# Kernel tuning notes

Measured on AMD Instinct MI355X. Metric: run time of the kernel, lower is better.

## Reference

```python
import jax, jax.numpy as jnp
import numpy as np

N = 8192
E = 262144
H = 64


def setup_inputs() -> dict:
    key = jax.random.key(0)
    ks = jax.random.split(key, 9)
    edge_index = jax.random.randint(ks[0], (2, E), 0, N, dtype=jnp.int64)
    edge_attr = jax.random.uniform(ks[1], (E,), dtype=jnp.float32)
    node_features = jax.random.normal(ks[2], (N, N), dtype=jnp.float32)
    # GCNConv weights (glorot-ish scale) and biases
    W1 = jax.random.normal(ks[3], (N, H), dtype=jnp.float32) / np.sqrt(N)
    b1 = jnp.zeros((H,), dtype=jnp.float32)
    W2 = jax.random.normal(ks[4], (H, H), dtype=jnp.float32) / np.sqrt(H)
    b2 = jnp.zeros((H,), dtype=jnp.float32)
    fcW = jax.random.normal(ks[5], (H, N), dtype=jnp.float32) / np.sqrt(H)
    fcb = jnp.zeros((N,), dtype=jnp.float32)
    return {"edge_index": edge_index, "edge_attr": edge_attr,
            "node_features": node_features,
            "W1": W1, "b1": b1, "W2": W2, "b2": b2,
            "fcW": fcW, "fcb": fcb}


def _gcn_conv(x, W, b, src, dst, ew, n_nodes):
    # PyG GCNConv with edge weights: x' = D^{-1/2} (A + I) D^{-1/2} (x W) + b
    # src/dst/ew already include self-loops (weight 1.0).
    x = x @ W                                        # [N, out]
    deg = jax.ops.segment_sum(ew, dst, num_segments=n_nodes)  # in-degree w/ loops
    dinv = jax.lax.rsqrt(deg)                        # deg >= 1 due to self loops
    norm = dinv[src] * ew * dinv[dst]                # [E+N]
    out = jax.ops.segment_sum(x[src] * norm[:, None], dst, num_segments=n_nodes)
    return out + b


def reference(edge_index, edge_attr, node_features, W1, b1, W2, b2, fcW, fcb):
    n_nodes = node_features.shape[0]
    loops = jnp.arange(n_nodes, dtype=edge_index.dtype)
    src = jnp.concatenate([edge_index[0], loops])
    dst = jnp.concatenate([edge_index[1], loops])
    ew = jnp.concatenate([edge_attr, jnp.ones((n_nodes,), edge_attr.dtype)])
    x = jax.nn.relu(_gcn_conv(node_features, W1, b1, src, dst, ew, n_nodes))
    x = jax.nn.relu(_gcn_conv(x, W2, b2, src, dst, ew, n_nodes))
    x = x @ fcW + fcb
    return jax.nn.softmax(x, axis=-1)
```

## Files before the change

### kernel.cpp

```cpp
#include <hip/hip_runtime.h>


#define NN 8192
#define NE 262144
#define HD 64
#define KCH 1024
#define NKC 8
#define NTS (KCH/64)

typedef float f32x4 __attribute__((ext_vector_type(4)));
typedef short v8s   __attribute__((ext_vector_type(8)));
typedef unsigned short ushort_t;

__device__ __forceinline__ unsigned short bf16_rne(float f){
  union { float f; unsigned u; } v; v.f = f;
  unsigned r = v.u + 0x7fffu + ((v.u >> 16) & 1u);
  return (unsigned short)(r >> 16);
}
__device__ __forceinline__ float bf16_f32(unsigned short h){
  union { unsigned u; float f; } v; v.u = ((unsigned)h) << 16;
  return v.f;
}
__device__ __forceinline__ f32x4 mfma16(v8s a, v8s b, f32x4 c){
  return __builtin_amdgcn_mfma_f32_16x16x32_bf16(a, b, c, 0, 0, 0);
}
__device__ __forceinline__ void gload16(const void* g, void* l){
  __builtin_amdgcn_global_load_lds(
      (const __attribute__((address_space(1))) unsigned int*)g,
      (__attribute__((address_space(3))) unsigned int*)l, 16, 0, 0);
}

__global__ __launch_bounds__(256) void k_xcast(const float* __restrict__ X,
                                               ushort_t* __restrict__ xb){
  size_t i = ((size_t)blockIdx.x*256 + threadIdx.x)*8;
  f32x4 a = *(const f32x4*)(X + i);
  f32x4 b = *(const f32x4*)(X + i + 4);
  v8s o;
  #pragma unroll
  for (int j=0;j<4;++j){
    o[j]   = (short)bf16_rne(a[j]);
    o[4+j] = (short)bf16_rne(b[j]);
  }
  *(v8s*)(xb + i) = o;
}

__global__ void k_prep0(const float* __restrict__ W1, const float* __restrict__ fcW,
                        ushort_t* w1hi, ushort_t* fcwp,
                        float* deg, int* cnt, int* wcnt, float* S){
  int idx = blockIdx.x*blockDim.x + threadIdx.x;
  if (idx < NN){ deg[idx]=1.0f; cnt[idx]=0; wcnt[idx]=0; S[idx]=0.0f; }
  {
    int kk = idx & 31, c = (idx>>5)&15, nt = (idx>>9)&3, kb = idx>>11;
    int k = kb*32 + kk, col = nt*16 + c;
    float w = W1[(size_t)k*HD + col];
    int chunk = idx >> 3, e = idx & 7;
    int sidx = ((chunk ^ (c & 7)) << 3) | e;
    w1hi[sidx] = bf16_rne(w);
  }
  {
    int kk = idx & 31, c = (idx>>5)&15, cblk = (idx>>9)&511, kb = idx>>18;
    int k = kb*32 + kk, col = cblk*16 + c;
    fcwp[idx] = bf16_rne(fcW[(size_t)k*NN + col]);
  }
}

__global__ void k_deg_cnt(const int* ei, const float* ew, float* deg, int* cnt){
  int e = blockIdx.x*blockDim.x + threadIdx.x;
  if (e < NE){
    int d = ei[NE + e];
    atomicAdd(&deg[d], ew[e]);
    atomicAdd(&cnt[d], 1);
  }
}

__global__ void k_scan(const int* cnt, const float* deg, int* rowptr, float* dinv){
  __shared__ int part[256];
  int t = threadIdx.x;
  int loc[32]; int s = 0;
  #pragma unroll
  for (int j=0;j<32;++j){ loc[j] = cnt[t*32+j]; s += loc[j]; }
  part[t] = s; __syncthreads();
  for (int off=1; off<256; off<<=1){
    int v = (t >= off) ? part[t-off] : 0;
    __syncthreads();
    part[t] += v;
    __syncthreads();
  }
  int run = part[t] - s;
  #pragma unroll
  for (int j=0;j<32;++j){ rowptr[t*32+j] = run; run += loc[j]; }
  if (t == 255) rowptr[NN] = run;
  #pragma unroll
  for (int j=0;j<32;++j) dinv[t*32+j] = 1.0f / sqrtf(deg[t*32+j]);
}

__global__ void k_fill(const int* ei, const float* ew, const float* dinv,
                       const int* rowptr, int* wcnt, int* csr_src, float* csr_nrm){
  int e = blockIdx.x*blockDim.x + threadIdx.x;
  if (e < NE){
    int s = ei[e], d = ei[NE+e];
    int slot = rowptr[d] + atomicAdd(&wcnt[d], 1);
    csr_src[slot] = s;
    csr_nrm[slot] = dinv[s] * ew[e] * dinv[d];
  }
}

__global__ __launch_bounds__(256, 4) void k_gemm1(const ushort_t* __restrict__ Xb,
                                                  const ushort_t* __restrict__ w1hi,
                                                  float* __restrict__ xw1p){
  __shared__ __align__(16) char sA[2][8192];
  __shared__ __align__(16) char sB[2][8192];
  int lane = threadIdx.x & 63, w = threadIdx.x >> 6;
  int r = lane & 15, seg = lane >> 4;
  int c8 = lane & 7, r8 = lane >> 3;
  int row0 = blockIdx.x*64, kb0 = blockIdx.y*KCH;

  const char* Xc  = (const char*)Xb;
  const char* w1c = (const char*)w1hi;
  size_t asrc[2];
  #pragma unroll
  for (int i=0;i<2;++i){
    int rl = w*16 + i*8 + r8;
    asrc[i] = (size_t)(row0 + rl)*(NN*2) + (size_t)kb0*2 + (size_t)((c8 ^ r8)*16);
  }

  int aoff[2];
  #pragma unroll
  for (int ks=0; ks<2; ++ks)
    aoff[ks] = (w*16 + r)*128 + (((ks*4 + seg) ^ (r & 7)) << 4);
  int bc[4];
  #pragma unroll
  for (int nt=0; nt<4; ++nt)
    bc[nt] = ((nt*64 + r*4 + seg) ^ (r & 7)) << 4;

  f32x4 z = {0.f,0.f,0.f,0.f};
  f32x4 acc[4] = {z,z,z,z};

  auto STAGE = [&](int t, int b){
    char* aD = (char*)sA[b] + w*2048;
    gload16(Xc + asrc[0] + (size_t)t*128, aD);
    gload16(Xc + asrc[1] + (size_t)t*128, aD + 1024);
    size_t sBo = ((size_t)(kb0 >> 5) + 2*t)*4096 + w*1024 + lane*16;
    gload16(w1c + sBo,        (char*)sB[b] + w*1024);
    gload16(w1c + sBo + 4096, (char*)sB[b] + 4096 + w*1024);
  };

  STAGE(0, 0);

  for (int t = 0; t < NTS; ++t){
    int cur = t & 1;
    if (t + 1 < NTS){
      STAGE(t+1, cur^1);
      asm volatile("s_waitcnt vmcnt(4)" ::: "memory");
    } else {
      asm volatile("s_waitcnt vmcnt(0)" ::: "memory");
    }
    __builtin_amdgcn_s_barrier();
    __builtin_amdgcn_sched_barrier(0);
    #pragma unroll
    for (int ks=0; ks<2; ++ks){
      v8s a = *(const v8s*)(&sA[cur][aoff[ks]]);
      #pragma unroll
      for (int nt=0; nt<4; ++nt){
        v8s b = *(const v8s*)(&sB[cur][ks*4096 + bc[nt]]);
        acc[nt] = mfma16(a, b, acc[nt]);
      }
    }
    __builtin_amdgcn_sched_barrier(0);
    __builtin_amdgcn_s_barrier();
  }

  float* o = xw1p + (size_t)blockIdx.y*(NN*HD) + (size_t)(row0 + w*16)*HD;
  #pragma unroll
  for (int nt=0; nt<4; ++nt)
    #pragma unroll
    for (int j=0;j<4;++j)
      o[(4*seg + j)*HD + nt*16 + r] = acc[nt][j];
}

__global__ __launch_bounds__(256) void k_red(const float* __restrict__ xw1p,
                                             float* __restrict__ xw1){
  int i = blockIdx.x*blockDim.x + threadIdx.x;
  f32x4 s = {0.f,0.f,0.f,0.f};
  #pragma unroll
  for (int c=0;c<NKC;++c){
    f32x4 v = *(const f32x4*)(xw1p + (size_t)c*NN*HD + (size_t)i*4);
    s[0]+=v[0]; s[1]+=v[1]; s[2]+=v[2]; s[3]+=v[3];
  }
  *(f32x4*)(xw1 + (size_t)i*4) = s;
}

__global__ __launch_bounds__(256) void k_agg1c(const float* __restrict__ xin,
                                               const float* __restrict__ b1,
                                               const float* __restrict__ W2,
                                               const float* __restrict__ dinv,
                                               const int* __restrict__ rowptr,
                                               const int* __restrict__ csr_src,
                                               const float* __restrict__ csr_nrm,
                                               float* __restrict__ x2w){
  __shared__ float W2s[64*64];
  __shared__ float rows[4][64];
  int lane = threadIdx.x & 63, w = threadIdx.x >> 6;
  for (int o = threadIdx.x; o < 64*64; o += 256) W2s[o] = W2[o];
  __syncthreads();

  int i = blockIdx.x*4 + w;
  float di = dinv[i];
  float acc = di*di * xin[(size_t)i*HD + lane];
  int e = rowptr[i], e1 = rowptr[i+1];
  for (; e + 1 < e1; e += 2){
    int s0 = csr_src[e], s1 = csr_src[e+1];
    float n0 = csr_nrm[e], n1 = csr_nrm[e+1];
    acc += n0 * xin[(size_t)s0*HD + lane];
    acc += n1 * xin[(size_t)s1*HD + lane];
  }
  if (e < e1) acc += csr_nrm[e] * xin[(size_t)csr_src[e]*HD + lane];
  float v = acc + b1[lane];
  rows[w][lane] = v > 0.f ? v : 0.f;
  __syncthreads();

  float acc2 = 0.f;
  #pragma unroll
  for (int k=0;k<64;++k) acc2 += rows[w][k] * W2s[k*64 + lane];
  x2w[(size_t)i*HD + lane] = acc2;
}

__global__ __launch_bounds__(256) void k_agg2(const float* __restrict__ xin,
                                              const float* __restrict__ b2,
                                              const float* __restrict__ dinv,
                                              const int* __restrict__ rowptr,
                                              const int* __restrict__ csr_src,
                                              const float* __restrict__ csr_nrm,
                                              ushort_t* __restrict__ x2b){
  int lane = threadIdx.x & 63, w = threadIdx.x >> 6;
  int i = blockIdx.x*4 + w;
  float di = dinv[i];
  float acc = di*di * xin[(size_t)i*HD + lane];
  int e = rowptr[i], e1 = rowptr[i+1];
  for (; e + 1 < e1; e += 2){
    int s0 = csr_src[e], s1 = csr_src[e+1];
    float n0 = csr_nrm[e], n1 = csr_nrm[e+1];
    acc += n0 * xin[(size_t)s0*HD + lane];
    acc += n1 * xin[(size_t)s1*HD + lane];
  }
  if (e < e1) acc += csr_nrm[e] * xin[(size_t)csr_src[e]*HD + lane];
  float v = acc + b2[lane];
  v = v > 0.f ? v : 0.f;
  x2b[(size_t)i*HD + lane] = bf16_rne(v);
}

__global__ __launch_bounds__(256) void k_rowsum(const ushort_t* __restrict__ x2b,
                                                const ushort_t* __restrict__ fcwp,
                                                const float* __restrict__ fcb,
                                                float* __restrict__ S){
  int lane = threadIdx.x & 63, w = threadIdx.x >> 6;
  int r = lane & 15, seg = lane >> 4;
  int row0 = blockIdx.x*128 + w*32;
  const ushort_t* xb = x2b + (size_t)(row0 + r)*HD + seg*8;
  v8s x00 = *(const v8s*)(xb);
  v8s x01 = *(const v8s*)(xb + 32);
  v8s x10 = *(const v8s*)(xb + 16*HD);
  v8s x11 = *(const v8s*)(xb + 16*HD + 32);
  float rp0 = 0.f, rp1 = 0.f;
  for (int cb=0; cb<4; ++cb){
    int colbase = blockIdx.y*256 + cb*64;
    f32x4 z = {0.f,0.f,0.f,0.f};
    f32x4 acc0[4] = {z,z,z,z}, acc1[4] = {z,z,z,z};
    #pragma unroll
    for (int nt=0; nt<4; ++nt){
      int cblk = (colbase >> 4) + nt;
      v8s bA = *(const v8s*)(fcwp + ((size_t)cblk*16 + r)*32 + seg*8);
      v8s bB = *(const v8s*)(fcwp + ((size_t)(512 + cblk)*16 + r)*32 + seg*8);
      acc0[nt] = mfma16(bA, x00, acc0[nt]);
      acc0[nt] = mfma16(bB, x01, acc0[nt]);
      acc1[nt] = mfma16(bA, x10, acc1[nt]);
      acc1[nt] = mfma16(bB, x11, acc1[nt]);
    }
    #pragma unroll
    for (int nt=0; nt<4; ++nt){
      int col = colbase + nt*16 + seg*4;
      f32x4 fb = *(const f32x4*)(fcb + col);
      #pragma unroll
      for (int j=0;j<4;++j){
        rp0 += __expf(acc0[nt][j] + fb[j]);
        rp1 += __expf(acc1[nt][j] + fb[j]);
      }
    }
  }
  rp0 += __shfl_xor(rp0, 16); rp0 += __shfl_xor(rp0, 32);
  rp1 += __shfl_xor(rp1, 16); rp1 += __shfl_xor(rp1, 32);
  if (lane < 16){
    atomicAdd(&S[row0 + lane],      rp0);
    atomicAdd(&S[row0 + 16 + lane], rp1);
  }
}

__global__ __launch_bounds__(256) void k_passB(const ushort_t* __restrict__ x2b,
                                               const ushort_t* __restrict__ fcwp,
                                               const float* __restrict__ fcb,
                                               const float* __restrict__ S,
                                               float* __restrict__ out){
  int lane = threadIdx.x & 63, w = threadIdx.x >> 6;
  int r = lane & 15, seg = lane >> 4;
  int row0 = blockIdx.x*128 + w*32;
  const ushort_t* xb = x2b + (size_t)(row0 + r)*HD + seg*8;
  v8s x00 = *(const v8s*)(xb);
  v8s x01 = *(const v8s*)(xb + 32);
  v8s x10 = *(const v8s*)(xb + 16*HD);
  v8s x11 = *(const v8s*)(xb + 16*HD + 32);
  float si0 = 1.0f / S[row0 + r];
  float si1 = 1.0f / S[row0 + 16 + r];
  float* o0 = out + (size_t)(row0 + r)*NN;
  float* o1 = out + (size_t)(row0 + 16 + r)*NN;
  for (int cb=0; cb<4; ++cb){
    int colbase = blockIdx.y*256 + cb*64;
    f32x4 z = {0.f,0.f,0.f,0.f};
    f32x4 acc0[4] = {z,z,z,z}, acc1[4] = {z,z,z,z};
    #pragma unroll
    for (int nt=0; nt<4; ++nt){
      int cblk = (colbase >> 4) + nt;
      v8s bA = *(const v8s*)(fcwp + ((size_t)cblk*16 + r)*32 + seg*8);
      v8s bB = *(const v8s*)(fcwp + ((size_t)(512 + cblk)*16 + r)*32 + seg*8);
      acc0[nt] = mfma16(bA, x00, acc0[nt]);
      acc0[nt] = mfma16(bB, x01, acc0[nt]);
      acc1[nt] = mfma16(bA, x10, acc1[nt]);
      acc1[nt] = mfma16(bB, x11, acc1[nt]);
    }
    #pragma unroll
    for (int nt=0; nt<4; ++nt){
      int col = colbase + nt*16 + seg*4;
      f32x4 fb = *(const f32x4*)(fcb + col);
      f32x4 v0, v1;
      #pragma unroll
      for (int j=0;j<4;++j){
        v0[j] = __expf(acc0[nt][j] + fb[j]) * si0;
        v1[j] = __expf(acc1[nt][j] + fb[j]) * si1;
      }
      *(f32x4*)(o0 + col) = v0;
      *(f32x4*)(o1 + col) = v1;
    }
  }
}

extern "C" void kernel_launch(void* const* d_in, const int* in_sizes, int n_in,
                              void* d_out, int out_size, void* d_ws, size_t ws_size,
                              hipStream_t stream){
  (void)in_sizes; (void)n_in; (void)out_size; (void)ws_size;
  const int*   ei  = (const int*)  d_in[0];
  const float* ew  = (const float*)d_in[1];
  const float* X   = (const float*)d_in[2];
  const float* W1  = (const float*)d_in[3];
  const float* b1  = (const float*)d_in[4];
  const float* W2  = (const float*)d_in[5];
  const float* b2  = (const float*)d_in[6];
  const float* fcW = (const float*)d_in[7];
  const float* fcb = (const float*)d_in[8];
  float* out = (float*)d_out;
  char*  ws  = (char*)d_ws;

  float*    deg     = (float*)   (ws + 0);
  float*    dinv    = (float*)   (ws + 32768);
  int*      cnt     = (int*)     (ws + 65536);
  int*      wcnt    = (int*)     (ws + 98304);
  int*      rowptr  = (int*)     (ws + 131072);
  int*      csr_src = (int*)     (ws + 167936);
  float*    csr_nrm = (float*)   (ws + 1216512);
  ushort_t* w1hi    = (ushort_t*)(ws + 2265088);
  ushort_t* fcwp    = (ushort_t*)(ws + 4362240);
  float*    xw1p    = (float*)   (ws + 5410816);
  float*    xw1     = (float*)   (ws + 22188032);
  float*    x2w     = (float*)   (ws + 24285184);
  ushort_t* x2b     = (ushort_t*)(ws + 26382336);
  float*    S       = (float*)   (ws + 27430912);

  ushort_t* Xbf = (ushort_t*)d_out;

  k_prep0   <<<2048,  256, 0, stream>>>(W1, fcW, w1hi, fcwp, deg, cnt, wcnt, S);
  k_xcast   <<<32768, 256, 0, stream>>>(X, Xbf);
  k_deg_cnt <<<1024,  256, 0, stream>>>(ei, ew, deg, cnt);
  k_scan    <<<1,     256, 0, stream>>>(cnt, deg, rowptr, dinv);
  k_fill    <<<1024,  256, 0, stream>>>(ei, ew, dinv, rowptr, wcnt, csr_src, csr_nrm);
  k_gemm1   <<<dim3(128, NKC), 256, 0, stream>>>(Xbf, w1hi, xw1p);
  k_red     <<<512,   256, 0, stream>>>(xw1p, xw1);
  k_agg1c   <<<2048,  256, 0, stream>>>(xw1, b1, W2, dinv, rowptr, csr_src, csr_nrm, x2w);
  k_agg2    <<<2048,  256, 0, stream>>>(x2w, b2, dinv, rowptr, csr_src, csr_nrm, x2b);
  k_rowsum  <<<dim3(64,32), 256, 0, stream>>>(x2b, fcwp, fcb, S);
  k_passB   <<<dim3(64,32), 256, 0, stream>>>(x2b, fcwp, fcb, S, out);
}
```

Measured before the change: 296.0 us.

## Pre-tile bf16 X into MFMA fragment layout so gemm1 loads are contiguous

The elementwise fp32-to-bf16 cast kernel is replaced by a cast-and-retile kernel. It stages 16x512 tiles in LDS and writes X in the exact per-lane MFMA fragment order that gemm1 consumes. gemm1 then loads A with fully contiguous 1 KB per-wave global-to-LDS copies and reads its fragments linearly, without the XOR swizzle and strided row addressing. The cast kernel gains an LDS round trip and a less regular write pattern, but total traffic stays the same.

```diff
diff --git a/kernel.cpp b/kernel.cpp
--- a/kernel.cpp
+++ b/kernel.cpp
@@ -30,18 +30,41 @@
       (__attribute__((address_space(3))) unsigned int*)l, 16, 0, 0);
 }
 
-__global__ __launch_bounds__(256) void k_xcast(const float* __restrict__ X,
-                                               ushort_t* __restrict__ xb){
-  size_t i = ((size_t)blockIdx.x*256 + threadIdx.x)*8;
-  f32x4 a = *(const f32x4*)(X + i);
-  f32x4 b = *(const f32x4*)(X + i + 4);
-  v8s o;
-  #pragma unroll
-  for (int j=0;j<4;++j){
-    o[j]   = (short)bf16_rne(a[j]);
-    o[4+j] = (short)bf16_rne(b[j]);
-  }
-  *(v8s*)(xb + i) = o;
+__global__ __launch_bounds__(256) void k_xt(const float* __restrict__ X,
+                                            ushort_t* __restrict__ Xt){
+  __shared__ ushort_t lds[16*520];
+  int t = threadIdx.x;
+  int bx = blockIdx.x, by = blockIdx.y;
+  int R0 = bx*16;
+  size_t K0 = (size_t)by*512;
+  #pragma unroll
+  for (int p=0;p<2;++p){
+    int rl = p*8 + (t>>5);
+    const float* src = X + (size_t)(R0 + rl)*NN + K0 + (size_t)(t&31)*16;
+    f32x4 v0 = *(const f32x4*)(src);
+    f32x4 v1 = *(const f32x4*)(src+4);
+    f32x4 v2 = *(const f32x4*)(src+8);
+    f32x4 v3 = *(const f32x4*)(src+12);
+    v8s o0, o1;
+    #pragma unroll
+    for (int j=0;j<4;++j){
+      o0[j] = (short)bf16_rne(v0[j]); o0[4+j] = (short)bf16_rne(v1[j]);
+      o1[j] = (short)bf16_rne(v2[j]); o1[4+j] = (short)bf16_rne(v3[j]);
+    }
+    ushort_t* d = lds + rl*520 + (t&31)*16;
+    *(v8s*)(d)   = o0;
+    *(v8s*)(d+8) = o1;
+  }
+  __syncthreads();
+  size_t outbase = ((size_t)bx*256 + (size_t)by*16)*512;
+  #pragma unroll
+  for (int c=0;c<4;++c){
+    int f = c*256 + t;
+    int kg_l = f >> 6, lane = f & 63;
+    int seg = lane >> 4, r = lane & 15;
+    v8s v = *(const v8s*)(lds + r*520 + kg_l*32 + seg*8);
+    *(v8s*)(Xt + outbase + (size_t)f*8) = v;
+  }
 }
 
 __global__ void k_prep0(const float* __restrict__ W1, const float* __restrict__ fcW,
@@ -105,29 +128,21 @@
   }
 }
 
-__global__ __launch_bounds__(256, 4) void k_gemm1(const ushort_t* __restrict__ Xb,
+__global__ __launch_bounds__(256, 4) void k_gemm1(const ushort_t* __restrict__ Xt,
                                                   const ushort_t* __restrict__ w1hi,
                                                   float* __restrict__ xw1p){
   __shared__ __align__(16) char sA[2][8192];
   __shared__ __align__(16) char sB[2][8192];
   int lane = threadIdx.x & 63, w = threadIdx.x >> 6;
   int r = lane & 15, seg = lane >> 4;
-  int c8 = lane & 7, r8 = lane >> 3;
   int row0 = blockIdx.x*64, kb0 = blockIdx.y*KCH;
-
-  const char* Xc  = (const char*)Xb;
+  int gtile = blockIdx.x*4 + w;
+  int kg0 = blockIdx.y*(KCH/32);
+
+  const char* Xc  = (const char*)Xt;
   const char* w1c = (const char*)w1hi;
-  size_t asrc[2];
-  #pragma unroll
-  for (int i=0;i<2;++i){
-    int rl = w*16 + i*8 + r8;
-    asrc[i] = (size_t)(row0 + rl)*(NN*2) + (size_t)kb0*2 + (size_t)((c8 ^ r8)*16);
-  }
-
-  int aoff[2];
-  #pragma unroll
-  for (int ks=0; ks<2; ++ks)
-    aoff[ks] = (w*16 + r)*128 + (((ks*4 + seg) ^ (r & 7)) << 4);
+  size_t abase = (((size_t)gtile*256 + kg0)*64 + lane)*16;
+
   int bc[4];
   #pragma unroll
   for (int nt=0; nt<4; ++nt)
@@ -137,9 +152,9 @@
   f32x4 acc[4] = {z,z,z,z};
 
   auto STAGE = [&](int t, int b){
-    char* aD = (char*)sA[b] + w*2048;
-    gload16(Xc + asrc[0] + (size_t)t*128, aD);
-    gload16(Xc + asrc[1] + (size_t)t*128, aD + 1024);
+    size_t aOff = abase + (size_t)t*2048;
+    gload16(Xc + aOff,        (char*)sA[b] + w*1024);
+    gload16(Xc + aOff + 1024, (char*)sA[b] + 4096 + w*1024);
     size_t sBo = ((size_t)(kb0 >> 5) + 2*t)*4096 + w*1024 + lane*16;
     gload16(w1c + sBo,        (char*)sB[b] + w*1024);
     gload16(w1c + sBo + 4096, (char*)sB[b] + 4096 + w*1024);
@@ -159,7 +174,7 @@
     __builtin_amdgcn_sched_barrier(0);
     #pragma unroll
     for (int ks=0; ks<2; ++ks){
-      v8s a = *(const v8s*)(&sA[cur][aoff[ks]]);
+      v8s a = *(const v8s*)(&sA[cur][ks*4096 + w*1024 + lane*16]);
       #pragma unroll
       for (int nt=0; nt<4; ++nt){
         v8s b = *(const v8s*)(&sB[cur][ks*4096 + bc[nt]]);
@@ -373,17 +388,17 @@
   ushort_t* x2b     = (ushort_t*)(ws + 26382336);
   float*    S       = (float*)   (ws + 27430912);
 
-  ushort_t* Xbf = (ushort_t*)d_out;
-
-  k_prep0   <<<2048,  256, 0, stream>>>(W1, fcW, w1hi, fcwp, deg, cnt, wcnt, S);
-  k_xcast   <<<32768, 256, 0, stream>>>(X, Xbf);
-  k_deg_cnt <<<1024,  256, 0, stream>>>(ei, ew, deg, cnt);
-  k_scan    <<<1,     256, 0, stream>>>(cnt, deg, rowptr, dinv);
-  k_fill    <<<1024,  256, 0, stream>>>(ei, ew, dinv, rowptr, wcnt, csr_src, csr_nrm);
-  k_gemm1   <<<dim3(128, NKC), 256, 0, stream>>>(Xbf, w1hi, xw1p);
-  k_red     <<<512,   256, 0, stream>>>(xw1p, xw1);
-  k_agg1c   <<<2048,  256, 0, stream>>>(xw1, b1, W2, dinv, rowptr, csr_src, csr_nrm, x2w);
-  k_agg2    <<<2048,  256, 0, stream>>>(x2w, b2, dinv, rowptr, csr_src, csr_nrm, x2b);
+  ushort_t* Xt = (ushort_t*)d_out;
+
+  k_prep0   <<<2048, 256, 0, stream>>>(W1, fcW, w1hi, fcwp, deg, cnt, wcnt, S);
+  k_xt      <<<dim3(512,16), 256, 0, stream>>>(X, Xt);
+  k_deg_cnt <<<1024, 256, 0, stream>>>(ei, ew, deg, cnt);
+  k_scan    <<<1,    256, 0, stream>>>(cnt, deg, rowptr, dinv);
+  k_fill    <<<1024, 256, 0, stream>>>(ei, ew, dinv, rowptr, wcnt, csr_src, csr_nrm);
+  k_gemm1   <<<dim3(128, NKC), 256, 0, stream>>>(Xt, w1hi, xw1p);
+  k_red     <<<512,  256, 0, stream>>>(xw1p, xw1);
+  k_agg1c   <<<2048, 256, 0, stream>>>(xw1, b1, W2, dinv, rowptr, csr_src, csr_nrm, x2w);
+  k_agg2    <<<2048, 256, 0, stream>>>(x2w, b2, dinv, rowptr, csr_src, csr_nrm, x2b);
   k_rowsum  <<<dim3(64,32), 256, 0, stream>>>(x2b, fcwp, fcb, S);
   k_passB   <<<dim3(64,32), 256, 0, stream>>>(x2b, fcwp, fcb, S, out);
 }
```

New measurement: 301.0 us. No clear change (+1.7%).
